# Optimization experiments

Measured on AMD Instinct MI355X. Metric: run time of the kernel, lower is better.

Reference implementation:

```python
import jax, jax.numpy as jnp
import numpy as np

B, S, F = 2, 2048, 2048
H, D = 16, 128  # F == H * D


def setup_inputs() -> dict:
    key = jax.random.key(0)
    k1, k2, k3 = jax.random.split(key, 3)
    x = jax.random.normal(k1, (B, S, F), dtype=jnp.float32)
    # causal attention mask, broadcast over batch and heads
    mask = jnp.tril(jnp.ones((S, S), dtype=bool))[None, None, :, :]
    init_std = 0.02
    c_attn_kernel = jax.random.normal(k2, (F, 3 * F), dtype=jnp.float32) * init_std
    c_attn_bias = jnp.zeros((3 * F,), dtype=jnp.float32)
    c_proj_kernel = jax.random.normal(k3, (F, F), dtype=jnp.float32) * init_std
    c_proj_bias = jnp.zeros((F,), dtype=jnp.float32)
    return {
        "x": x,
        "mask": mask,
        "c_attn_kernel": c_attn_kernel,
        "c_attn_bias": c_attn_bias,
        "c_proj_kernel": c_proj_kernel,
        "c_proj_bias": c_proj_bias,
    }


def reference(x, mask, c_attn_kernel, c_attn_bias, c_proj_kernel, c_proj_bias):
    dtype = x.dtype
    # fused QKV projection: [B,S,F] @ [F,3F] -> [B,S,3F]
    hidden = jnp.einsum('bsf,fe->bse', x, c_attn_kernel) + c_attn_bias
    q, k, v = jnp.split(hidden, 3, axis=-1)
    split = lambda t: t.reshape(t.shape[:-1] + (H, D))  # [B,S,H,D]
    q, k, v = split(q), split(k), split(v)
    q = q / jnp.sqrt(jnp.asarray(D, dtype))
    scores = jnp.einsum('bqhd,bkhd->bhqk', q, k)  # [B,H,S,S]
    big_neg = jnp.finfo(dtype).min
    scores = jnp.where(mask[..., :S, :S], scores, big_neg)
    weights = jax.nn.softmax(scores, axis=-1)
    z = jnp.einsum('bhqk,bkhd->bqhd', weights, v)  # [B,S,H,D]
    merged = z.reshape(z.shape[:-2] + (F,))  # [B,S,F]
    out = jnp.einsum('bsf,fe->bse', merged, c_proj_kernel) + c_proj_bias
    return out
```

## Files before the change

kernel.cpp:

```cpp
#include <hip/hip_runtime.h>
#include <hip/hip_bf16.h>
#include <stdint.h>

typedef __attribute__((ext_vector_type(8))) __bf16 bf16x8;
typedef __attribute__((ext_vector_type(4))) __bf16 bf16x4;
typedef __attribute__((ext_vector_type(4))) float f32x4;

#define DEV __device__ __forceinline__

static constexpr int S = 2048, F = 2048, H = 16, D = 128;
static constexpr int KDIM = F;
static constexpr float QSCALE = 0.08838834764831845f;

DEV void gll16(const void* g, void* l) {
  __builtin_amdgcn_global_load_lds(
      (const __attribute__((address_space(1))) void*)g,
      (__attribute__((address_space(3))) void*)l, 16, 0, 0);
}

DEV f32x4 mfma16(bf16x8 a, bf16x8 b, f32x4 c) {
  return __builtin_amdgcn_mfma_f32_16x16x32_bf16(a, b, c, 0, 0, 0);
}

extern __shared__ char smem[];

#define QBAR()  __builtin_amdgcn_s_barrier()
#define QLGKM() asm volatile("s_waitcnt lgkmcnt(0)" ::: "memory")
#define QSCB()  __builtin_amdgcn_sched_barrier(0)

__global__ void k_prep(const float* __restrict__ x, __bf16* __restrict__ xb,
                       const float* __restrict__ wa, __bf16* __restrict__ wat,
                       const float* __restrict__ wp, __bf16* __restrict__ wpt) {
  __shared__ float t[64][65];
  const int bid = blockIdx.x;
  if (bid < 8192) {
    int i = bid * 256 + threadIdx.x;
    float4 v = reinterpret_cast<const float4*>(x)[i];
    bf16x4 o = {(__bf16)v.x, (__bf16)v.y, (__bf16)v.z, (__bf16)v.w};
    reinterpret_cast<bf16x4*>(xb)[i] = o;
    return;
  }
  const float* in;
  __bf16* out;
  int rows, cols, c0, r0;
  if (bid < 11264) {
    int tb = bid - 8192;
    in = wa; out = wat; rows = 2048; cols = 6144;
    c0 = (tb % 96) * 64; r0 = (tb / 96) * 64;
  } else {
    int tb = bid - 11264;
    in = wp; out = wpt; rows = 2048; cols = 2048;
    c0 = (tb % 32) * 64; r0 = (tb / 32) * 64;
  }
  const int tx = threadIdx.x & 63, ty = threadIdx.x >> 6;
#pragma unroll
  for (int i = 0; i < 64; i += 4)
    t[ty + i][tx] = in[(size_t)(r0 + ty + i) * cols + c0 + tx];
  __syncthreads();
#pragma unroll
  for (int i = 0; i < 64; i += 4)
    out[(size_t)(c0 + ty + i) * rows + r0 + tx] = (__bf16)t[tx][ty + i];
}

__global__ __launch_bounds__(512, 1) void k_qkv8p(
    const __bf16* __restrict__ A, const __bf16* __restrict__ Bt,
    const float* __restrict__ bias,
    __bf16* __restrict__ qo, __bf16* __restrict__ ko, __bf16* __restrict__ vo) {
  constexpr int NT = 32;
  const int tid = threadIdx.x;
  const int lane = tid & 63, wid = tid >> 6;
  const int wm = wid >> 2, wn = wid & 3;
  const int ln = lane & 15, lm = lane >> 4;

  const int lin = (blockIdx.x & 7) * 64 + (blockIdx.x >> 3);
  const int by = lin >> 4, bx = lin & 15;
  const int mBase = by * 128, nBase = bx * 384;

  const int r0 = tid >> 3, cc = tid & 7;
  const int src0 = r0 * KDIM + ((cc ^ (r0 & 7)) << 3);
  const __bf16* Ab = A + (size_t)mBase * KDIM + src0;
  const __bf16* Bb = Bt + (size_t)nBase * KDIM + src0;
  const int sDst = wid * 1024;

  auto stA2 = [&](int t) {
    char* d = smem + (t & 1) * 65536 + sDst;
    const __bf16* s = Ab + t * 64;
    gll16(s, d);
    gll16(s + (size_t)64 * KDIM, d + 8192);
  };
  auto stB2 = [&](int t, int j) {
    char* d = smem + (t & 1) * 65536 + 16384 + j * 8192 + sDst;
    const __bf16* s = Bb + (size_t)j * 64 * KDIM + t * 64;
    gll16(s, d);
    gll16(s + (size_t)64 * KDIM, d + 8192);
  };

  int rA[2], rB[2];
#pragma unroll
  for (int ks = 0; ks < 2; ++ks) {
    const int slot = (ks * 4 + lm) ^ (ln & 7);
    rA[ks] = (wm * 64 + ln) * 128 + slot * 16;
    rB[ks] = 16384 + (wn * 96 + ln) * 128 + slot * 16;
  }
  auto rdA = [&](bf16x8 (&a)[4], const char* cb, int ks) {
#pragma unroll
    for (int mi = 0; mi < 4; ++mi)
      a[mi] = *reinterpret_cast<const bf16x8*>(cb + rA[ks] + mi * 2048);
  };
  auto rdBh = [&](bf16x8 (&b)[3], const char* cb, int ks, int h) {
#pragma unroll
    for (int k = 0; k < 3; ++k)
      b[k] = *reinterpret_cast<const bf16x8*>(cb + rB[ks] + (h * 3 + k) * 2048);
  };

  f32x4 acc[4][6] = {};
  auto mm = [&](const bf16x8 (&a)[4], const bf16x8 (&b)[3], int h) {
#pragma unroll
    for (int k = 0; k < 3; ++k)
#pragma unroll
      for (int mi = 0; mi < 4; ++mi)
        acc[mi][h * 3 + k] = mfma16(a[mi], b[k], acc[mi][h * 3 + k]);
  };

  stA2(0); stB2(0, 0); stB2(0, 2); stB2(0, 4); stA2(1);
  asm volatile("s_waitcnt vmcnt(2)" ::: "memory");
  QBAR(); QSCB();

  for (int i = 0; i < 16; ++i) {
    const char* L = smem;
    const char* R = smem + 65536;
    const int tR = 2 * i + 1, tN = 2 * i + 2, tN1 = 2 * i + 3;
    const bool last = (i == 15);
    bf16x8 a[4], b[3];

    rdA(a, L, 0); rdBh(b, L, 0, 0);
    stB2(tR, 0);
    QBAR(); QLGKM(); QSCB();
    __builtin_amdgcn_s_setprio(1); mm(a, b, 0); __builtin_amdgcn_s_setprio(0);
    QBAR(); QSCB();
    rdBh(b, L, 0, 1);
    stB2(tR, 2);
    QBAR(); QLGKM(); QSCB();
    __builtin_amdgcn_s_setprio(1); mm(a, b, 1); __builtin_amdgcn_s_setprio(0);
    QBAR(); QSCB();
    rdA(a, L, 1); rdBh(b, L, 1, 1);
    stB2(tR, 4);
    QBAR(); QLGKM(); QSCB();
    __builtin_amdgcn_s_setprio(1); mm(a, b, 1); __builtin_amdgcn_s_setprio(0);
    QBAR(); QSCB();
    rdBh(b, L, 1, 0);
    if (!last) stA2(tN);
    QBAR(); QLGKM(); QSCB();
    __builtin_amdgcn_s_setprio(1); mm(a, b, 0); __builtin_amdgcn_s_setprio(0);
    if (last) asm volatile("s_waitcnt vmcnt(0)" ::: "memory");
    else      asm volatile("s_waitcnt vmcnt(2)" ::: "memory");
    QBAR(); QSCB();

    rdA(a, R, 0); rdBh(b, R, 0, 0);
    if (!last) stB2(tN, 0);
    QBAR(); QLGKM(); QSCB();
    __builtin_amdgcn_s_setprio(1); mm(a, b, 0); __builtin_amdgcn_s_setprio(0);
    QBAR(); QSCB();
    rdBh(b, R, 0, 1);
    if (!last) stB2(tN, 2);
    QBAR(); QLGKM(); QSCB();
    __builtin_amdgcn_s_setprio(1); mm(a, b, 1); __builtin_amdgcn_s_setprio(0);
    QBAR(); QSCB();
    rdA(a, R, 1); rdBh(b, R, 1, 1);
    if (!last) stB2(tN, 4);
    QBAR(); QLGKM(); QSCB();
    __builtin_amdgcn_s_setprio(1); mm(a, b, 1); __builtin_amdgcn_s_setprio(0);
    QBAR(); QSCB();
    rdBh(b, R, 1, 0);
    if (tN1 < NT) stA2(tN1);
    QBAR(); QLGKM(); QSCB();
    __builtin_amdgcn_s_setprio(1); mm(a, b, 0); __builtin_amdgcn_s_setprio(0);
    if (!last) {
      asm volatile("s_waitcnt vmcnt(2)" ::: "memory");
      QBAR(); QSCB();
    }
  }

#pragma unroll
  for (int mi = 0; mi < 4; ++mi) {
    const int grow = mBase + wm * 64 + mi * 16 + lm * 4;
    const int b = grow >> 11, s0 = grow & 2047;
#pragma unroll
    for (int ni = 0; ni < 6; ++ni) {
      const int gcol = nBase + wn * 96 + ni * 16 + ln;
      const float bv = bias[gcol];
      const int sec = gcol >> 11;
      const int h = (gcol >> 7) & 15, d = gcol & 127;
      const int bh = b * H + h;
      if (sec == 0) {
#pragma unroll
        for (int r = 0; r < 4; ++r)
          qo[((size_t)bh * S + s0 + r) * D + d] = (__bf16)((acc[mi][ni][r] + bv) * QSCALE);
      } else if (sec == 1) {
#pragma unroll
        for (int r = 0; r < 4; ++r)
          ko[((size_t)bh * S + s0 + r) * D + d] = (__bf16)(acc[mi][ni][r] + bv);
      } else {
        bf16x4 pv = {(__bf16)(acc[mi][ni][0] + bv), (__bf16)(acc[mi][ni][1] + bv),
                     (__bf16)(acc[mi][ni][2] + bv), (__bf16)(acc[mi][ni][3] + bv)};
        *reinterpret_cast<bf16x4*>(vo + ((size_t)bh * D + d) * S + s0) = pv;
      }
    }
  }
}

__global__ __launch_bounds__(512, 1) void k_proj(
    const __bf16* __restrict__ A, const __bf16* __restrict__ Bt,
    const float* __restrict__ bias, float* __restrict__ fo) {
  constexpr int BM = 128, BN = 256;
  constexpr int MF = 4, NF = 4, NH = 2;
  constexpr int AOFF = BM * 128;
  constexpr int BUFSZ = (BM + BN) * 128;
  constexpr int NT = KDIM / 64;

  const int tid = threadIdx.x;
  const int lane = tid & 63, wid = tid >> 6;
  const int wm = wid >> 2, wn = wid & 3;
  const int ln = lane & 15, lm = lane >> 4;

  const int lin = (blockIdx.x & 7) * 32 + (blockIdx.x >> 3);
  const int by = lin >> 3, bx = lin & 7;
  const int mBase = by * BM, nBase = bx * BN;

  const int r0 = tid >> 3, cc = tid & 7;
  const int src0 = r0 * KDIM + ((cc ^ (r0 & 7)) << 3);
  const __bf16* Ab = A + (size_t)mBase * KDIM + src0;
  const __bf16* Bb = Bt + (size_t)nBase * KDIM + src0;
  const int dstBase = wid * 1024;

  auto stage = [&](char* buf, int t) {
    const __bf16* As = Ab + t * 64;
    const __bf16* Bs = Bb + t * 64;
#pragma unroll
    for (int j = 0; j < 2; ++j)
      gll16(As + (size_t)j * 64 * KDIM, buf + j * 8192 + dstBase);
#pragma unroll
    for (int j = 0; j < 4; ++j)
      gll16(Bs + (size_t)j * 64 * KDIM, buf + AOFF + j * 8192 + dstBase);
  };

  int rA[2], rB[2];
#pragma unroll
  for (int ks = 0; ks < 2; ++ks) {
    const int slot = (ks * 4 + lm) ^ (ln & 7);
    rA[ks] = (wm * 64 + ln) * 128 + slot * 16;
    rB[ks] = AOFF + (wn * 64 + ln) * 128 + slot * 16;
  }

  f32x4 acc[MF][NF] = {};

  stage(smem, 0);
  stage(smem + BUFSZ, 1);
  asm volatile("s_waitcnt vmcnt(6)" ::: "memory");
  QBAR(); QSCB();

  for (int t = 0; t < NT; ++t) {
    char* cb = smem + (t & 1) * BUFSZ;
    bf16x8 a0[MF], a1[MF], b0[NF], b1[NF];

#pragma unroll
    for (int mi = 0; mi < MF; ++mi)
      a0[mi] = *reinterpret_cast<const bf16x8*>(cb + rA[0] + mi * 2048);
#pragma unroll
    for (int ni = 0; ni < NF; ++ni)
      b0[ni] = *reinterpret_cast<const bf16x8*>(cb + rB[0] + ni * 2048);

    __builtin_amdgcn_s_setprio(1);
#pragma unroll
    for (int ni = 0; ni < NH; ++ni)
#pragma unroll
      for (int mi = 0; mi < MF; ++mi)
        acc[mi][ni] = mfma16(a0[mi], b0[ni], acc[mi][ni]);
    __builtin_amdgcn_s_setprio(0);

#pragma unroll
    for (int mi = 0; mi < MF; ++mi)
      a1[mi] = *reinterpret_cast<const bf16x8*>(cb + rA[1] + mi * 2048);
#pragma unroll
    for (int ni = NH; ni < NF; ++ni)
      b1[ni] = *reinterpret_cast<const bf16x8*>(cb + rB[1] + ni * 2048);

    __builtin_amdgcn_s_setprio(1);
#pragma unroll
    for (int ni = NH; ni < NF; ++ni)
#pragma unroll
      for (int mi = 0; mi < MF; ++mi)
        acc[mi][ni] = mfma16(a0[mi], b0[ni], acc[mi][ni]);
    __builtin_amdgcn_s_setprio(0);

#pragma unroll
    for (int ni = 0; ni < NH; ++ni)
      b1[ni] = *reinterpret_cast<const bf16x8*>(cb + rB[1] + ni * 2048);

    __builtin_amdgcn_s_setprio(1);
#pragma unroll
    for (int ni = NH; ni < NF; ++ni)
#pragma unroll
      for (int mi = 0; mi < MF; ++mi)
        acc[mi][ni] = mfma16(a1[mi], b1[ni], acc[mi][ni]);
    __builtin_amdgcn_s_setprio(0);

    QLGKM();
    QBAR(); QSCB();
    if (t + 2 < NT) stage(cb, t + 2);

    __builtin_amdgcn_s_setprio(1);
#pragma unroll
    for (int ni = 0; ni < NH; ++ni)
#pragma unroll
      for (int mi = 0; mi < MF; ++mi)
        acc[mi][ni] = mfma16(a1[mi], b1[ni], acc[mi][ni]);
    __builtin_amdgcn_s_setprio(0);

    if (t + 2 < NT) {
      asm volatile("s_waitcnt vmcnt(6)" ::: "memory");
    } else if (t + 1 < NT) {
      asm volatile("s_waitcnt vmcnt(0)" ::: "memory");
    }
    if (t + 1 < NT) {
      QBAR(); QSCB();
    }
  }

#pragma unroll
  for (int mi = 0; mi < MF; ++mi) {
    const int grow = mBase + wm * 64 + mi * 16 + lm * 4;
#pragma unroll
    for (int ni = 0; ni < NF; ++ni) {
      const int gcol = nBase + wn * 64 + ni * 16 + ln;
      const float bv = bias[gcol];
#pragma unroll
      for (int r = 0; r < 4; ++r)
        fo[(size_t)(grow + r) * F + gcol] = acc[mi][ni][r] + bv;
    }
  }
}

__global__ __launch_bounds__(256, 2) void k_attn(
    const __bf16* __restrict__ qb, const __bf16* __restrict__ kb,
    const __bf16* __restrict__ vtb, __bf16* __restrict__ zb) {
  const int lane = threadIdx.x & 63, w = threadIdx.x >> 6;
  const int lm = lane >> 4, ln = lane & 15;
  const int blk = blockIdx.x;
  const int u = blk & 255, v = blk >> 8;
  const int qt = v ? (u >> 4) : 15 - (u >> 4);
  const int bh = ((u & 15) << 1) | v;
  const int qw = qt * 128 + w * 32;

  const __bf16* qp = qb + (size_t)bh * S * D;
  const __bf16* kp = kb + (size_t)bh * S * D;
  const __bf16* vp = vtb + (size_t)bh * D * S;
  char* pw = smem + 65536 + w * 4096;

  int ksrc[4], kdst[4], vsrc[4], vdst[4];
#pragma unroll
  for (int j = 0; j < 4; ++j) {
    int c = (w * 4 + j) * 64 + lane;
    int kr = c >> 4, kps = (c & 15) ^ (kr & 7);
    ksrc[j] = kr * D + kps * 8;
    kdst[j] = (w * 4 + j) * 1024;
    int vr = c >> 3, vps = (c & 7) ^ (vr & 7);
    vsrc[j] = vr * S + vps * 8;
    vdst[j] = 16384 + (w * 4 + j) * 1024;
  }
  auto stage = [&](int kt) {
    char* buf = smem + (kt & 1) * 32768;
    const int kv = kt * 64;
#pragma unroll
    for (int j = 0; j < 4; ++j) gll16(kp + (size_t)kv * D + ksrc[j], buf + kdst[j]);
#pragma unroll
    for (int j = 0; j < 4; ++j) gll16(vp + kv + vsrc[j], buf + vdst[j]);
  };

  bf16x8 qf[2][4];
#pragma unroll
  for (int mi = 0; mi < 2; ++mi)
#pragma unroll
    for (int kf = 0; kf < 4; ++kf)
      qf[mi][kf] = *reinterpret_cast<const bf16x8*>(qp + (qw + mi * 16 + ln) * D + kf * 32 + lm * 8);

  f32x4 Oa[2][8] = {};
  float mrow[2][4], lrow[2][4];
#pragma unroll
  for (int mi = 0; mi < 2; ++mi)
#pragma unroll
    for (int r = 0; r < 4; ++r) { mrow[mi][r] = -3.0e38f; lrow[mi][r] = 0.0f; }

  const int ktEnd = 2 * qt + 1;

  stage(0);
  stage(1);
  asm volatile("s_waitcnt vmcnt(8)" ::: "memory");
  QBAR(); QSCB();

  for (int kt = 0; kt <= ktEnd; ++kt) {
    const int kv0 = kt * 64;
    const int cur = kt & 1;
    const char* Kb = smem + cur * 32768;
    const char* Vb = Kb + 16384;

    if (kv0 <= qw + 31) {
      const bool diag = (kv0 + 63 > qw);

      f32x4 sacc[2][4] = {};
#pragma unroll
      for (int kf = 0; kf < 4; ++kf) {
        bf16x8 kfr[4];
#pragma unroll
        for (int ni = 0; ni < 4; ++ni) {
          int row = ni * 16 + ln;
          int ch = (kf * 4 + lm) ^ (row & 7);
          kfr[ni] = *reinterpret_cast<const bf16x8*>(Kb + row * 256 + ch * 16);
        }
        __builtin_amdgcn_s_setprio(1);
#pragma unroll
        for (int mi = 0; mi < 2; ++mi)
#pragma unroll
          for (int ni = 0; ni < 4; ++ni)
            sacc[mi][ni] = mfma16(qf[mi][kf], kfr[ni], sacc[mi][ni]);
        __builtin_amdgcn_s_setprio(0);
      }

      if (diag) {
#pragma unroll
        for (int ni = 0; ni < 4; ++ni) {
          int c = kv0 + ni * 16 + ln;
#pragma unroll
          for (int mi = 0; mi < 2; ++mi) {
            int q0r = qw + mi * 16 + lm * 4;
#pragma unroll
            for (int r = 0; r < 4; ++r)
              if (c > q0r + r) sacc[mi][ni][r] = -1e30f;
          }
        }
      }

      float lmax[2][4];
      bool big = false;
#pragma unroll
      for (int mi = 0; mi < 2; ++mi)
#pragma unroll
        for (int r = 0; r < 4; ++r) {
          float m4 = fmaxf(fmaxf(sacc[mi][0][r], sacc[mi][1][r]),
                           fmaxf(sacc[mi][2][r], sacc[mi][3][r]));
          lmax[mi][r] = m4;
          big = big || (m4 > mrow[mi][r] + 8.0f);
        }
      if (__any((int)big)) {
#pragma unroll
        for (int mi = 0; mi < 2; ++mi)
#pragma unroll
          for (int r = 0; r < 4; ++r) {
            float mx = lmax[mi][r];
            mx = fmaxf(mx, __shfl_xor(mx, 1, 64));
            mx = fmaxf(mx, __shfl_xor(mx, 2, 64));
            mx = fmaxf(mx, __shfl_xor(mx, 4, 64));
            mx = fmaxf(mx, __shfl_xor(mx, 8, 64));
            float mnew = fmaxf(mrow[mi][r], mx);
            float corr = __expf(mrow[mi][r] - mnew);
            mrow[mi][r] = mnew;
            lrow[mi][r] *= corr;
#pragma unroll
            for (int ni = 0; ni < 8; ++ni) Oa[mi][ni][r] *= corr;
          }
      }
#pragma unroll
      for (int mi = 0; mi < 2; ++mi)
#pragma unroll
        for (int r = 0; r < 4; ++r) {
          float rs = 0.0f;
#pragma unroll
          for (int ni = 0; ni < 4; ++ni) {
            float p = __expf(sacc[mi][ni][r] - mrow[mi][r]);
            sacc[mi][ni][r] = p;
            rs += p;
          }
          lrow[mi][r] += rs;
        }

#pragma unroll
      for (int mi = 0; mi < 2; ++mi)
#pragma unroll
        for (int ni = 0; ni < 4; ++ni)
#pragma unroll
          for (int r = 0; r < 4; ++r) {
            int row = mi * 16 + lm * 4 + r;
            int bo = (row * 128 + (ni * 16 + ln) * 2) ^ ((row & 7) << 4);
            *reinterpret_cast<__bf16*>(pw + bo) = (__bf16)sacc[mi][ni][r];
          }

      QLGKM(); QSCB();

#pragma unroll
      for (int kf = 0; kf < 2; ++kf) {
        bf16x8 pfr[2], vfr[8];
#pragma unroll
        for (int mi = 0; mi < 2; ++mi) {
          int row = mi * 16 + ln;
          int ch = (kf * 4 + lm) ^ (row & 7);
          pfr[mi] = *reinterpret_cast<const bf16x8*>(pw + row * 128 + ch * 16);
        }
#pragma unroll
        for (int ni = 0; ni < 8; ++ni) {
          int row = ni * 16 + ln;
          int ch = (kf * 4 + lm) ^ (row & 7);
          vfr[ni] = *reinterpret_cast<const bf16x8*>(Vb + row * 128 + ch * 16);
        }
        __builtin_amdgcn_s_setprio(1);
#pragma unroll
        for (int mi = 0; mi < 2; ++mi)
#pragma unroll
          for (int ni = 0; ni < 8; ++ni)
            Oa[mi][ni] = mfma16(pfr[mi], vfr[ni], Oa[mi][ni]);
        __builtin_amdgcn_s_setprio(0);
      }
    }

    asm volatile("s_waitcnt lgkmcnt(0)" ::: "memory");
    QBAR(); QSCB();
    if (kt + 2 <= ktEnd) stage(kt + 2);
    if (kt + 1 <= ktEnd) {
      if (kt + 2 <= ktEnd)
        asm volatile("s_waitcnt vmcnt(8)" ::: "memory");
      else
        asm volatile("s_waitcnt vmcnt(0)" ::: "memory");
      QBAR(); QSCB();
    }
  }

#pragma unroll
  for (int mi = 0; mi < 2; ++mi)
#pragma unroll
    for (int r = 0; r < 4; ++r) {
      float ls = lrow[mi][r];
      ls += __shfl_xor(ls, 1, 64);
      ls += __shfl_xor(ls, 2, 64);
      ls += __shfl_xor(ls, 4, 64);
      ls += __shfl_xor(ls, 8, 64);
      lrow[mi][r] = 1.0f / ls;
    }
  const int b = bh >> 4, h = bh & 15;
#pragma unroll
  for (int mi = 0; mi < 2; ++mi)
#pragma unroll
    for (int ni = 0; ni < 8; ++ni) {
      int d = ni * 16 + ln;
#pragma unroll
      for (int r = 0; r < 4; ++r) {
        int qrow = qw + mi * 16 + lm * 4 + r;
        zb[(size_t)(b * S + qrow) * F + h * D + d] = (__bf16)(Oa[mi][ni][r] * lrow[mi][r]);
      }
    }
}

extern "C" void kernel_launch(void* const* d_in, const int* in_sizes, int n_in,
                              void* d_out, int out_size, void* d_ws, size_t ws_size,
                              hipStream_t stream) {
  const float* x = (const float*)d_in[0];
  const float* w_attn = (const float*)d_in[2];
  const float* b_attn = (const float*)d_in[3];
  const float* w_proj = (const float*)d_in[4];
  const float* b_proj = (const float*)d_in[5];
  float* out = (float*)d_out;

  char* ws = (char*)d_ws;
  __bf16* xb    = (__bf16*)(ws + 0);
  __bf16* wqkv  = (__bf16*)(ws + 16777216);
  __bf16* wpro  = (__bf16*)(ws + 41943040);
  __bf16* qb    = (__bf16*)(ws + 50331648);
  __bf16* kb    = (__bf16*)(ws + 67108864);
  __bf16* vtb   = (__bf16*)(ws + 83886080);
  __bf16* zb    = xb;

  (void)hipFuncSetAttribute((const void*)k_qkv8p,
                            hipFuncAttributeMaxDynamicSharedMemorySize, 131072);
  (void)hipFuncSetAttribute((const void*)k_proj,
                            hipFuncAttributeMaxDynamicSharedMemorySize, 98304);
  (void)hipFuncSetAttribute((const void*)k_attn,
                            hipFuncAttributeMaxDynamicSharedMemorySize, 81920);

  k_prep<<<12288, 256, 0, stream>>>(x, xb, w_attn, wqkv, w_proj, wpro);
  k_qkv8p<<<512, 512, 131072, stream>>>(xb, wqkv, b_attn, qb, kb, vtb);
  k_attn<<<512, 256, 81920, stream>>>(qb, kb, vtb, zb);
  k_proj<<<256, 512, 98304, stream>>>(zb, wpro, b_proj, out);
}
```

Before: 235.4 us.

## Port output projection GEMM to the 8-phase interleaved pipeline schedule

Rewrites the output projection kernel to use the same 8-phase schedule as the QKV GEMM. Each K step is split into four sub-phases, and the prefetch loads for the next tiles are interleaved between the LDS reads and MFMA groups. Waits are tuned to vmcnt(2), with barriers around each phase. The aim is to hide global-to-LDS latency better and keep the matrix units busy, at the cost of many more barriers per iteration.

```diff
diff --git a/kernel.cpp b/kernel.cpp
--- a/kernel.cpp
+++ b/kernel.cpp
@@ -138,16 +138,19 @@
     QBAR(); QLGKM(); QSCB();
     __builtin_amdgcn_s_setprio(1); mm(a, b, 0); __builtin_amdgcn_s_setprio(0);
     QBAR(); QSCB();
+
     rdBh(b, L, 0, 1);
     stB2(tR, 2);
     QBAR(); QLGKM(); QSCB();
     __builtin_amdgcn_s_setprio(1); mm(a, b, 1); __builtin_amdgcn_s_setprio(0);
     QBAR(); QSCB();
+
     rdA(a, L, 1); rdBh(b, L, 1, 1);
     stB2(tR, 4);
     QBAR(); QLGKM(); QSCB();
     __builtin_amdgcn_s_setprio(1); mm(a, b, 1); __builtin_amdgcn_s_setprio(0);
     QBAR(); QSCB();
+
     rdBh(b, L, 1, 0);
     if (!last) stA2(tN);
     QBAR(); QLGKM(); QSCB();
@@ -161,16 +164,19 @@
     QBAR(); QLGKM(); QSCB();
     __builtin_amdgcn_s_setprio(1); mm(a, b, 0); __builtin_amdgcn_s_setprio(0);
     QBAR(); QSCB();
+
     rdBh(b, R, 0, 1);
     if (!last) stB2(tN, 2);
     QBAR(); QLGKM(); QSCB();
     __builtin_amdgcn_s_setprio(1); mm(a, b, 1); __builtin_amdgcn_s_setprio(0);
     QBAR(); QSCB();
+
     rdA(a, R, 1); rdBh(b, R, 1, 1);
     if (!last) stB2(tN, 4);
     QBAR(); QLGKM(); QSCB();
     __builtin_amdgcn_s_setprio(1); mm(a, b, 1); __builtin_amdgcn_s_setprio(0);
     QBAR(); QSCB();
+
     rdBh(b, R, 1, 0);
     if (tN1 < NT) stA2(tN1);
     QBAR(); QLGKM(); QSCB();
@@ -209,15 +215,10 @@
   }
 }
 
-__global__ __launch_bounds__(512, 1) void k_proj(
+__global__ __launch_bounds__(512, 1) void k_proj8p(
     const __bf16* __restrict__ A, const __bf16* __restrict__ Bt,
     const float* __restrict__ bias, float* __restrict__ fo) {
-  constexpr int BM = 128, BN = 256;
-  constexpr int MF = 4, NF = 4, NH = 2;
-  constexpr int AOFF = BM * 128;
-  constexpr int BUFSZ = (BM + BN) * 128;
-  constexpr int NT = KDIM / 64;
-
+  constexpr int NT = 32;
   const int tid = threadIdx.x;
   const int lane = tid & 63, wid = tid >> 6;
   const int wm = wid >> 2, wn = wid & 3;
@@ -225,23 +226,25 @@
 
   const int lin = (blockIdx.x & 7) * 32 + (blockIdx.x >> 3);
   const int by = lin >> 3, bx = lin & 7;
-  const int mBase = by * BM, nBase = bx * BN;
+  const int mBase = by * 128, nBase = bx * 256;
 
   const int r0 = tid >> 3, cc = tid & 7;
   const int src0 = r0 * KDIM + ((cc ^ (r0 & 7)) << 3);
   const __bf16* Ab = A + (size_t)mBase * KDIM + src0;
   const __bf16* Bb = Bt + (size_t)nBase * KDIM + src0;
-  const int dstBase = wid * 1024;
-
-  auto stage = [&](char* buf, int t) {
-    const __bf16* As = Ab + t * 64;
-    const __bf16* Bs = Bb + t * 64;
-#pragma unroll
-    for (int j = 0; j < 2; ++j)
-      gll16(As + (size_t)j * 64 * KDIM, buf + j * 8192 + dstBase);
-#pragma unroll
-    for (int j = 0; j < 4; ++j)
-      gll16(Bs + (size_t)j * 64 * KDIM, buf + AOFF + j * 8192 + dstBase);
+  const int sDst = wid * 1024;
+
+  auto stA2 = [&](int t) {
+    char* d = smem + (t & 1) * 49152 + sDst;
+    const __bf16* s = Ab + t * 64;
+    gll16(s, d);
+    gll16(s + (size_t)64 * KDIM, d + 8192);
+  };
+  auto stB2 = [&](int t, int j) {
+    char* d = smem + (t & 1) * 49152 + 16384 + j * 8192 + sDst;
+    const __bf16* s = Bb + (size_t)j * 64 * KDIM + t * 64;
+    gll16(s, d);
+    gll16(s + (size_t)64 * KDIM, d + 8192);
   };
 
   int rA[2], rB[2];
@@ -249,89 +252,90 @@
   for (int ks = 0; ks < 2; ++ks) {
     const int slot = (ks * 4 + lm) ^ (ln & 7);
     rA[ks] = (wm * 64 + ln) * 128 + slot * 16;
-    rB[ks] = AOFF + (wn * 64 + ln) * 128 + slot * 16;
-  }
-
-  f32x4 acc[MF][NF] = {};
-
-  stage(smem, 0);
-  stage(smem + BUFSZ, 1);
-  asm volatile("s_waitcnt vmcnt(6)" ::: "memory");
+    rB[ks] = 16384 + (wn * 64 + ln) * 128 + slot * 16;
+  }
+  auto rdA = [&](bf16x8 (&a)[4], const char* cb, int ks) {
+#pragma unroll
+    for (int mi = 0; mi < 4; ++mi)
+      a[mi] = *reinterpret_cast<const bf16x8*>(cb + rA[ks] + mi * 2048);
+  };
+  auto rdBh = [&](bf16x8 (&b)[2], const char* cb, int ks, int h) {
+#pragma unroll
+    for (int k = 0; k < 2; ++k)
+      b[k] = *reinterpret_cast<const bf16x8*>(cb + rB[ks] + (h * 2 + k) * 2048);
+  };
+
+  f32x4 acc[4][4] = {};
+  auto mm = [&](const bf16x8 (&a)[4], const bf16x8 (&b)[2], int h) {
+#pragma unroll
+    for (int k = 0; k < 2; ++k)
+#pragma unroll
+      for (int mi = 0; mi < 4; ++mi)
+        acc[mi][h * 2 + k] = mfma16(a[mi], b[k], acc[mi][h * 2 + k]);
+  };
+
+  stA2(0); stB2(0, 0); stB2(0, 2); stA2(1);
+  asm volatile("s_waitcnt vmcnt(2)" ::: "memory");
   QBAR(); QSCB();
 
-  for (int t = 0; t < NT; ++t) {
-    char* cb = smem + (t & 1) * BUFSZ;
-    bf16x8 a0[MF], a1[MF], b0[NF], b1[NF];
-
-#pragma unroll
-    for (int mi = 0; mi < MF; ++mi)
-      a0[mi] = *reinterpret_cast<const bf16x8*>(cb + rA[0] + mi * 2048);
-#pragma unroll
-    for (int ni = 0; ni < NF; ++ni)
-      b0[ni] = *reinterpret_cast<const bf16x8*>(cb + rB[0] + ni * 2048);
-
-    __builtin_amdgcn_s_setprio(1);
-#pragma unroll
-    for (int ni = 0; ni < NH; ++ni)
-#pragma unroll
-      for (int mi = 0; mi < MF; ++mi)
-        acc[mi][ni] = mfma16(a0[mi], b0[ni], acc[mi][ni]);
-    __builtin_amdgcn_s_setprio(0);
-
-#pragma unroll
-    for (int mi = 0; mi < MF; ++mi)
-      a1[mi] = *reinterpret_cast<const bf16x8*>(cb + rA[1] + mi * 2048);
-#pragma unroll
-    for (int ni = NH; ni < NF; ++ni)
-      b1[ni] = *reinterpret_cast<const bf16x8*>(cb + rB[1] + ni * 2048);
-
-    __builtin_amdgcn_s_setprio(1);
-#pragma unroll
-    for (int ni = NH; ni < NF; ++ni)
-#pragma unroll
-      for (int mi = 0; mi < MF; ++mi)
-        acc[mi][ni] = mfma16(a0[mi], b0[ni], acc[mi][ni]);
-    __builtin_amdgcn_s_setprio(0);
-
-#pragma unroll
-    for (int ni = 0; ni < NH; ++ni)
-      b1[ni] = *reinterpret_cast<const bf16x8*>(cb + rB[1] + ni * 2048);
-
-    __builtin_amdgcn_s_setprio(1);
-#pragma unroll
-    for (int ni = NH; ni < NF; ++ni)
-#pragma unroll
-      for (int mi = 0; mi < MF; ++mi)
-        acc[mi][ni] = mfma16(a1[mi], b1[ni], acc[mi][ni]);
-    __builtin_amdgcn_s_setprio(0);
-
-    QLGKM();
-    QBAR(); QSCB();
-    if (t + 2 < NT) stage(cb, t + 2);
-
-    __builtin_amdgcn_s_setprio(1);
-#pragma unroll
-    for (int ni = 0; ni < NH; ++ni)
-#pragma unroll
-      for (int mi = 0; mi < MF; ++mi)
-        acc[mi][ni] = mfma16(a1[mi], b1[ni], acc[mi][ni]);
-    __builtin_amdgcn_s_setprio(0);
-
-    if (t + 2 < NT) {
-      asm volatile("s_waitcnt vmcnt(6)" ::: "memory");
-    } else if (t + 1 < NT) {
-      asm volatile("s_waitcnt vmcnt(0)" ::: "memory");
-    }
-    if (t + 1 < NT) {
+  for (int i = 0; i < 16; ++i) {
+    const char* L = smem;
+    const char* R = smem + 49152;
+    const int tR = 2 * i + 1, tN = 2 * i + 2, tN1 = 2 * i + 3;
+    const bool last = (i == 15);
+    bf16x8 a[4], b[2];
+
+    rdA(a, L, 0); rdBh(b, L, 0, 0);
+    stB2(tR, 0);
+    QBAR(); QLGKM(); QSCB();
+    __builtin_amdgcn_s_setprio(1); mm(a, b, 0); __builtin_amdgcn_s_setprio(0);
+    QBAR(); QSCB();
+    rdBh(b, L, 0, 1);
+    stB2(tR, 2);
+    QBAR(); QLGKM(); QSCB();
+    __builtin_amdgcn_s_setprio(1); mm(a, b, 1); __builtin_amdgcn_s_setprio(0);
+    QBAR(); QSCB();
+    rdA(a, L, 1); rdBh(b, L, 1, 1);
+    if (!last) stA2(tN);
+    QBAR(); QLGKM(); QSCB();
+    __builtin_amdgcn_s_setprio(1); mm(a, b, 1); __builtin_amdgcn_s_setprio(0);
+    QBAR(); QSCB();
+    rdBh(b, L, 1, 0);
+    QBAR(); QLGKM(); QSCB();
+    __builtin_amdgcn_s_setprio(1); mm(a, b, 0); __builtin_amdgcn_s_setprio(0);
+    if (last) asm volatile("s_waitcnt vmcnt(0)" ::: "memory");
+    else      asm volatile("s_waitcnt vmcnt(2)" ::: "memory");
+    QBAR(); QSCB();
+
+    rdA(a, R, 0); rdBh(b, R, 0, 0);
+    if (!last) stB2(tN, 0);
+    QBAR(); QLGKM(); QSCB();
+    __builtin_amdgcn_s_setprio(1); mm(a, b, 0); __builtin_amdgcn_s_setprio(0);
+    QBAR(); QSCB();
+    rdBh(b, R, 0, 1);
+    if (!last) stB2(tN, 2);
+    QBAR(); QLGKM(); QSCB();
+    __builtin_amdgcn_s_setprio(1); mm(a, b, 1); __builtin_amdgcn_s_setprio(0);
+    QBAR(); QSCB();
+    rdA(a, R, 1); rdBh(b, R, 1, 1);
+    if (tN1 < NT) stA2(tN1);
+    QBAR(); QLGKM(); QSCB();
+    __builtin_amdgcn_s_setprio(1); mm(a, b, 1); __builtin_amdgcn_s_setprio(0);
+    QBAR(); QSCB();
+    rdBh(b, R, 1, 0);
+    QBAR(); QLGKM(); QSCB();
+    __builtin_amdgcn_s_setprio(1); mm(a, b, 0); __builtin_amdgcn_s_setprio(0);
+    if (!last) {
+      asm volatile("s_waitcnt vmcnt(2)" ::: "memory");
       QBAR(); QSCB();
     }
   }
 
 #pragma unroll
-  for (int mi = 0; mi < MF; ++mi) {
+  for (int mi = 0; mi < 4; ++mi) {
     const int grow = mBase + wm * 64 + mi * 16 + lm * 4;
 #pragma unroll
-    for (int ni = 0; ni < NF; ++ni) {
+    for (int ni = 0; ni < 4; ++ni) {
       const int gcol = nBase + wn * 64 + ni * 16 + ln;
       const float bv = bias[gcol];
 #pragma unroll
@@ -579,7 +583,7 @@
 
   (void)hipFuncSetAttribute((const void*)k_qkv8p,
                             hipFuncAttributeMaxDynamicSharedMemorySize, 131072);
-  (void)hipFuncSetAttribute((const void*)k_proj,
+  (void)hipFuncSetAttribute((const void*)k_proj8p,
                             hipFuncAttributeMaxDynamicSharedMemorySize, 98304);
   (void)hipFuncSetAttribute((const void*)k_attn,
                             hipFuncAttributeMaxDynamicSharedMemorySize, 81920);
@@ -587,5 +591,5 @@
   k_prep<<<12288, 256, 0, stream>>>(x, xb, w_attn, wqkv, w_proj, wpro);
   k_qkv8p<<<512, 512, 131072, stream>>>(xb, wqkv, b_attn, qb, kb, vtb);
   k_attn<<<512, 256, 81920, stream>>>(qb, kb, vtb, zb);
-  k_proj<<<256, 512, 98304, stream>>>(zb, wpro, b_proj, out);
-}
+  k_proj8p<<<256, 512, 98304, stream>>>(zb, wpro, b_proj, out);
+}
```

Result: no change. 233.4 us (-0.8%).
